# Kernel optimization log

Measured on AMD Instinct MI355X. Metric: run time of the kernel, lower is better.

The kernel has to match this reference:

```python
import jax, jax.numpy as jnp
import numpy as np
import math
from functools import partial

B = 256
H = 256
HEADS = 4
DK = H // HEADS
NA_MAX, NP_MAX, NH_MAX = 127, 23, 11


def _counts():
    i = np.arange(B)
    ac = (64 + i % 64).astype(np.int32)   # atoms per graph, 64..127
    pc = (8 + i % 16).astype(np.int32)    # pharm fragments per graph, 8..23
    hc = (4 + i % 8).astype(np.int32)     # hyper-edges per graph, 4..11
    return ac, pc, hc


def setup_inputs() -> dict:
    key = jax.random.key(0)
    ks = jax.random.split(key, 32)
    ac, pc, hc = _counts()
    na, npm, nh = int(ac.sum()), int(pc.sum()), int(hc.sum())
    w = 1.0 / math.sqrt(H)
    inp = {
        'atom_message': jax.random.normal(ks[0], (na, H), jnp.float32),
        'pharm_message': jax.random.normal(ks[1], (npm, H), jnp.float32),
        'hyper_message': jax.random.normal(ks[2], (nh, H), jnp.float32),
        'atom_counts': jnp.asarray(ac),
        'pharm_counts': jnp.asarray(pc),
        'hyper_counts': jnp.asarray(hc),
    }
    # two MultiHeadedAttention blocks: q/k/v/out linears each (W stored as [in, out])
    names = []
    for pre in ('p2h', 'a2p'):
        for part in ('Wq', 'bq', 'Wk', 'bk', 'Wv', 'bv', 'Wo', 'bo'):
            names.append(f'{pre}_{part}')
    ki = 3
    for n in names:
        if n.split('_')[1].startswith('W'):
            inp[n] = jax.random.normal(ks[ki], (H, H), jnp.float32) * w
        else:
            inp[n] = jax.random.normal(ks[ki], (H,), jnp.float32) * 0.01
        ki += 1
    # bidirectional GRU params, torch layout: W_ih [3H, H], W_hh [3H, H], b [3H]
    for d in ('f', 'b'):
        inp[f'gru_Wih_{d}'] = jax.random.normal(ks[ki], (3 * H, H), jnp.float32) * w; ki += 1
        inp[f'gru_Whh_{d}'] = jax.random.normal(ks[ki], (3 * H, H), jnp.float32) * w; ki += 1
        inp[f'gru_bih_{d}'] = jax.random.normal(ks[ki], (3 * H,), jnp.float32) * 0.01; ki += 1
        inp[f'gru_bhh_{d}'] = jax.random.normal(ks[ki], (3 * H,), jnp.float32) * 0.01; ki += 1
    return inp


def _split_pad(msg, counts, max_n):
    # faithful vectorized version of split_batch: narrow + zero-pad per graph
    starts = jnp.concatenate([jnp.zeros((1,), jnp.int32), jnp.cumsum(counts)[:-1].astype(jnp.int32)])
    j = jnp.arange(max_n)
    valid = j[None, :] < counts[:, None]                       # [B, max_n]
    idx = jnp.where(valid, starts[:, None] + j[None, :], msg.shape[0])
    padded_src = jnp.concatenate([msg, jnp.zeros((1, msg.shape[1]), msg.dtype)], 0)
    return padded_src[idx], valid                              # [B, max_n, H]


def _mha(q, k, v, mask, Wq, bq, Wk, bk, Wv, bv, Wo, bo):
    Bq, Lq, _ = q.shape
    def proj(x, W, b):
        y = x @ W + b
        return y.reshape(x.shape[0], x.shape[1], HEADS, DK).transpose(0, 2, 1, 3)
    qh, kh, vh = proj(q, Wq, bq), proj(k, Wk, bk), proj(v, Wv, bv)
    scores = jnp.einsum('bhqd,bhkd->bhqk', qh, kh) / math.sqrt(DK)
    scores = jnp.where(mask[:, None], jnp.float32(-1e9), scores)
    p = jax.nn.softmax(scores, axis=-1)
    o = jnp.einsum('bhqk,bhkd->bhqd', p, vh)
    o = o.transpose(0, 2, 1, 3).reshape(Bq, Lq, H)
    return o @ Wo + bo


def _gru_dir(x, h0, Wih, Whh, bih, bhh):
    # x: [B, T, H], torch GRU cell equations
    def step(h, xt):
        gi = xt @ Wih.T + bih
        gh = h @ Whh.T + bhh
        ir, iz, inn = jnp.split(gi, 3, axis=-1)
        hr, hz, hn = jnp.split(gh, 3, axis=-1)
        r = jax.nn.sigmoid(ir + hr)
        z = jax.nn.sigmoid(iz + hz)
        n = jnp.tanh(inn + r * hn)
        h = (1.0 - z) * n + z * h
        return h, h
    _, ys = jax.lax.scan(step, h0, x.transpose(1, 0, 2))
    return ys.transpose(1, 0, 2)


def reference(atom_message, pharm_message, hyper_message,
              p2h_Wq, p2h_bq, p2h_Wk, p2h_bk, p2h_Wv, p2h_bv, p2h_Wo, p2h_bo,
              a2p_Wq, a2p_bq, a2p_Wk, a2p_bk, a2p_Wv, a2p_bv, a2p_Wo, a2p_bo,
              gru_Wih_f, gru_Whh_f, gru_bih_f, gru_bhh_f,
              gru_Wih_b, gru_Whh_b, gru_bih_b, gru_bhh_b,
              atom_counts, pharm_counts, hyper_counts):
    atom_f, atom_valid = _split_pad(atom_message, atom_counts, NA_MAX)
    pharm_f, _ = _split_pad(pharm_message, pharm_counts, NP_MAX)
    hyper_f, _ = _split_pad(hyper_message, hyper_counts, NH_MAX)

    nz = lambda t: (t != 0).astype(jnp.float32)
    mask1 = jnp.einsum('bqh,bkh->bqk', nz(pharm_f), nz(hyper_f)) == 0  # [B, Np, Nh]
    mask2 = jnp.einsum('bqh,bkh->bqk', nz(atom_f), nz(pharm_f)) == 0   # [B, Na, Np]

    pharm_f = _mha(pharm_f, hyper_f, hyper_f, mask1,
                   p2h_Wq, p2h_bq, p2h_Wk, p2h_bk, p2h_Wv, p2h_bv, p2h_Wo, p2h_bo) + pharm_f
    h = _mha(atom_f, pharm_f, pharm_f, mask2,
             a2p_Wq, a2p_bq, a2p_Wk, a2p_bk, a2p_Wv, a2p_bv, a2p_Wo, a2p_bo) + atom_f

    h0 = h.max(axis=1)  # initial hidden per direction
    hf = _gru_dir(h, h0, gru_Wih_f, gru_Whh_f, gru_bih_f, gru_bhh_f)
    hb = _gru_dir(h[:, ::-1], h0, gru_Wih_b, gru_Whh_b, gru_bih_b, gru_bhh_b)[:, ::-1]
    hcat = jnp.concatenate([hf, hb], axis=-1)  # [B, Na, 2H]

    v = atom_valid.astype(hcat.dtype)[..., None]
    graph_embed = (hcat * v).sum(axis=1) / atom_counts[:, None].astype(hcat.dtype)
    return graph_embed  # [B, 2H]
```

## Files before the change

### kernel.cpp

```cpp
#include <hip/hip_runtime.h>
#include <hip/hip_fp16.h>
#include <math.h>

#define NB 256
#define HDIM 256
#define NHEADS 4
#define DKH 64
#define LA 127
#define LP 23
#define LH 11

typedef _Float16 h2v __attribute__((ext_vector_type(2)));
typedef _Float16 f16x8 __attribute__((ext_vector_type(8)));
typedef float f32x4 __attribute__((ext_vector_type(4)));
union F4H { float4 f4; h2v h[4]; };

__device__ __forceinline__ float dot2acc(h2v a, h2v b, float c) {
#if __has_builtin(__builtin_amdgcn_fdot2)
  return __builtin_amdgcn_fdot2(a, b, c, false);
#else
  return c + (float)a[0] * (float)b[0] + (float)a[1] * (float)b[1];
#endif
}

__device__ __forceinline__ float sigm(float x) { return 1.0f / (1.0f + __expf(-x)); }
__device__ __forceinline__ float tanh_fast(float x) { return 2.0f / (1.0f + __expf(-2.0f * x)) - 1.0f; }

__global__ void k_scan(const int* __restrict__ ac, const int* __restrict__ pc,
                       const int* __restrict__ hc, int* __restrict__ sa,
                       int* __restrict__ sp, int* __restrict__ sh) {
  int t = threadIdx.x;
  if (t == 0) { int s = 0; for (int i = 0; i < NB; i++) { sa[i] = s; s += ac[i]; } }
  else if (t == 1) { int s = 0; for (int i = 0; i < NB; i++) { sp[i] = s; s += pc[i]; } }
  else if (t == 2) { int s = 0; for (int i = 0; i < NB; i++) { sh[i] = s; s += hc[i]; } }
}

__global__ void k_cvt2(const float* __restrict__ a, __half* __restrict__ oa,
                       const float* __restrict__ b, __half* __restrict__ ob, int n) {
  int i = blockIdx.x * blockDim.x + threadIdx.x;
  if (i < n) oa[i] = __float2half(a[i]);
  else if (i < 2 * n) ob[i - n] = __float2half(b[i - n]);
}

__global__ void k_wprep2(const float* __restrict__ srcA, __half* __restrict__ dstA,
                         const float* __restrict__ srcB, __half* __restrict__ dstB) {
  const int NT = 768 * 256;
  int d0 = blockIdx.x * blockDim.x + threadIdx.x;
  const float* src = d0 < NT ? srcA : srcB;
  __half* dst = d0 < NT ? dstA : dstB;
  int d = d0 < NT ? d0 : d0 - NT;
  if (d0 >= 2 * NT) return;
  int u = d & 7;
  int lg = (d >> 3) & 3;
  int c = (d >> 5) % 768;
  int k0b = (d >> 5) / 768;
  dst[d] = __float2half(src[(size_t)c * 256 + k0b * 32 + lg * 8 + u]);
}

template <bool GATHER_A, bool RES_GATHER>
__global__ __launch_bounds__(256) void k_gemm(
    const float* __restrict__ A, const float* __restrict__ msg,
    const int* __restrict__ starts, const int* __restrict__ counts, int L,
    const float* __restrict__ W, const float* __restrict__ bias,
    const float* __restrict__ resmsg, float* __restrict__ C,
    __half* __restrict__ Ch, int N) {
  const int K = HDIM;
  __shared__ float As[16][76];
  __shared__ float Ws[16][72];
  int tid = threadIdx.x;
  int row0 = blockIdx.x * 64, col0 = blockIdx.y * 64;
  int arow = row0 + (tid >> 2);
  const float* asrc;
  if constexpr (GATHER_A) {
    int b = arow / L, t = arow - b * L;
    asrc = (t < counts[b]) ? (msg + (size_t)(starts[b] + t) * K) : nullptr;
  } else {
    asrc = A + (size_t)arow * K;
  }
  int ak = (tid & 3) * 4;
  int wk = tid >> 4, wn = (tid & 15) * 4;
  int ty = tid >> 4, tx = tid & 15;
  float acc[4][4] = {};
  for (int k0 = 0; k0 < K; k0 += 16) {
    float4 av = make_float4(0.f, 0.f, 0.f, 0.f);
    if (asrc) av = *(const float4*)(asrc + k0 + ak);
    float4 wv = *(const float4*)(W + (size_t)(k0 + wk) * N + col0 + wn);
    __syncthreads();
    int m = tid >> 2;
    As[ak + 0][m] = av.x; As[ak + 1][m] = av.y;
    As[ak + 2][m] = av.z; As[ak + 3][m] = av.w;
    *(float4*)&Ws[wk][wn] = wv;
    __syncthreads();
#pragma unroll
    for (int kk = 0; kk < 16; kk++) {
      float4 a = *(const float4*)&As[kk][ty * 4];
      float4 b = *(const float4*)&Ws[kk][tx * 4];
      acc[0][0] += a.x * b.x; acc[0][1] += a.x * b.y; acc[0][2] += a.x * b.z; acc[0][3] += a.x * b.w;
      acc[1][0] += a.y * b.x; acc[1][1] += a.y * b.y; acc[1][2] += a.y * b.z; acc[1][3] += a.y * b.w;
      acc[2][0] += a.z * b.x; acc[2][1] += a.z * b.y; acc[2][2] += a.z * b.z; acc[2][3] += a.z * b.w;
      acc[3][0] += a.w * b.x; acc[3][1] += a.w * b.y; acc[3][2] += a.w * b.z; acc[3][3] += a.w * b.w;
    }
  }
  float4 bv = *(const float4*)(bias + col0 + tx * 4);
#pragma unroll
  for (int i = 0; i < 4; i++) {
    int r = row0 + ty * 4 + i;
    float o0 = acc[i][0] + bv.x, o1 = acc[i][1] + bv.y,
          o2 = acc[i][2] + bv.z, o3 = acc[i][3] + bv.w;
    if constexpr (RES_GATHER) {
      int b = r / L, t = r - b * L;
      if (t < counts[b]) {
        float4 rv = *(const float4*)(resmsg + (size_t)(starts[b] + t) * K + col0 + tx * 4);
        o0 += rv.x; o1 += rv.y; o2 += rv.z; o3 += rv.w;
      }
    }
    size_t o = (size_t)r * N + col0 + tx * 4;
    *(float4*)(C + o) = make_float4(o0, o1, o2, o3);
    if (Ch) {
      Ch[o] = __float2half(o0); Ch[o + 1] = __float2half(o1);
      Ch[o + 2] = __float2half(o2); Ch[o + 3] = __float2half(o3);
    }
  }
}

template <bool GATHER_A>
__global__ __launch_bounds__(256) void k_gemm_kv(
    const float* __restrict__ A, const float* __restrict__ msg,
    const int* __restrict__ starts, const int* __restrict__ counts, int L,
    const float* __restrict__ W0, const float* __restrict__ b0, float* __restrict__ C0,
    const float* __restrict__ W1, const float* __restrict__ b1, float* __restrict__ C1) {
  const int K = HDIM, N = HDIM;
  const float* W = blockIdx.z ? W1 : W0;
  const float* bias = blockIdx.z ? b1 : b0;
  float* C = blockIdx.z ? C1 : C0;
  __shared__ float As[16][76];
  __shared__ float Ws[16][72];
  int tid = threadIdx.x;
  int row0 = blockIdx.x * 64, col0 = blockIdx.y * 64;
  int arow = row0 + (tid >> 2);
  const float* asrc;
  if constexpr (GATHER_A) {
    int b = arow / L, t = arow - b * L;
    asrc = (t < counts[b]) ? (msg + (size_t)(starts[b] + t) * K) : nullptr;
  } else {
    asrc = A + (size_t)arow * K;
  }
  int ak = (tid & 3) * 4;
  int wk = tid >> 4, wn = (tid & 15) * 4;
  int ty = tid >> 4, tx = tid & 15;
  float acc[4][4] = {};
  for (int k0 = 0; k0 < K; k0 += 16) {
    float4 av = make_float4(0.f, 0.f, 0.f, 0.f);
    if (asrc) av = *(const float4*)(asrc + k0 + ak);
    float4 wv = *(const float4*)(W + (size_t)(k0 + wk) * N + col0 + wn);
    __syncthreads();
    int m = tid >> 2;
    As[ak + 0][m] = av.x; As[ak + 1][m] = av.y;
    As[ak + 2][m] = av.z; As[ak + 3][m] = av.w;
    *(float4*)&Ws[wk][wn] = wv;
    __syncthreads();
#pragma unroll
    for (int kk = 0; kk < 16; kk++) {
      float4 a = *(const float4*)&As[kk][ty * 4];
      float4 b = *(const float4*)&Ws[kk][tx * 4];
      acc[0][0] += a.x * b.x; acc[0][1] += a.x * b.y; acc[0][2] += a.x * b.z; acc[0][3] += a.x * b.w;
      acc[1][0] += a.y * b.x; acc[1][1] += a.y * b.y; acc[1][2] += a.y * b.z; acc[1][3] += a.y * b.w;
      acc[2][0] += a.z * b.x; acc[2][1] += a.z * b.y; acc[2][2] += a.z * b.z; acc[2][3] += a.z * b.w;
      acc[3][0] += a.w * b.x; acc[3][1] += a.w * b.y; acc[3][2] += a.w * b.z; acc[3][3] += a.w * b.w;
    }
  }
  float4 bv = *(const float4*)(bias + col0 + tx * 4);
#pragma unroll
  for (int i = 0; i < 4; i++) {
    int r = row0 + ty * 4 + i;
    size_t o = (size_t)r * N + col0 + tx * 4;
    *(float4*)(C + o) = make_float4(acc[i][0] + bv.x, acc[i][1] + bv.y,
                                    acc[i][2] + bv.z, acc[i][3] + bv.w);
  }
}

__global__ __launch_bounds__(256) void k_mfma_gi2(
    const __half* __restrict__ A16,
    const __half* __restrict__ Wf_f, const __half* __restrict__ Wf_b,
    const float* __restrict__ bias_f, const float* __restrict__ bias_b,
    __half* __restrict__ Out_f, __half* __restrict__ Out_b) {
  const int N = 768;
  int y = blockIdx.y;
  const __half* Wf = y < 12 ? Wf_f : Wf_b;
  const float* bias = y < 12 ? bias_f : bias_b;
  __half* Out = y < 12 ? Out_f : Out_b;
  int col0 = (y < 12 ? y : y - 12) * 64;
  int w = threadIdx.x >> 6, l = threadIdx.x & 63;
  int row0 = blockIdx.x * 64 + w * 16;
  int lr = l & 15, lg = l >> 4;
  f32x4 acc[4] = {};
  const __half* arow = A16 + (size_t)(row0 + lr) * 256 + lg * 8;
#pragma unroll
  for (int k0b = 0; k0b < 8; k0b++) {
    f16x8 a = *(const f16x8*)(arow + k0b * 32);
#pragma unroll
    for (int nt = 0; nt < 4; nt++) {
      int c = col0 + nt * 16 + lr;
      f16x8 b = *(const f16x8*)(Wf + ((size_t)(k0b * N + c) * 4 + lg) * 8);
      acc[nt] = __builtin_amdgcn_mfma_f32_16x16x32_f16(a, b, acc[nt], 0, 0, 0);
    }
  }
#pragma unroll
  for (int nt = 0; nt < 4; nt++) {
    int c = col0 + nt * 16 + lr;
    float bv = bias[c];
#pragma unroll
    for (int r = 0; r < 4; r++) {
      int row = row0 + lg * 4 + r;
      Out[(size_t)row * N + c] = __float2half(acc[nt][r] + bv);
    }
  }
}

template <int LQ, int LK>
__global__ __launch_bounds__(128) void k_attn(
    float* __restrict__ q, const float* __restrict__ kbuf,
    const float* __restrict__ vbuf, const int* __restrict__ cq,
    const int* __restrict__ ck) {
  __shared__ float qs[LQ][65];
  __shared__ float ks[LK][65];
  __shared__ float vs[LK][65];
  int b = blockIdx.x, head = blockIdx.y;
  int tid = threadIdx.x;
  for (int idx = tid; idx < LQ * 16; idx += 128) {
    int i = idx >> 4, c = (idx & 15) * 4;
    float4 v = *(const float4*)(q + (size_t)(b * LQ + i) * HDIM + head * DKH + c);
    qs[i][c] = v.x; qs[i][c + 1] = v.y; qs[i][c + 2] = v.z; qs[i][c + 3] = v.w;
  }
  for (int idx = tid; idx < LK * 16; idx += 128) {
    int i = idx >> 4, c = (idx & 15) * 4;
    float4 v = *(const float4*)(kbuf + (size_t)(b * LK + i) * HDIM + head * DKH + c);
    ks[i][c] = v.x; ks[i][c + 1] = v.y; ks[i][c + 2] = v.z; ks[i][c + 3] = v.w;
    float4 w = *(const float4*)(vbuf + (size_t)(b * LK + i) * HDIM + head * DKH + c);
    vs[i][c] = w.x; vs[i][c + 1] = w.y; vs[i][c + 2] = w.z; vs[i][c + 3] = w.w;
  }
  __syncthreads();
  int nq = cq[b], nk = ck[b];
  for (int i = tid; i < LQ; i += 128) {
    float s[LK];
    float mx = -INFINITY;
    bool qv = i < nq;
#pragma unroll
    for (int k = 0; k < LK; k++) {
      float d = -1e9f;
      if (qv && k < nk) {
        float acc = 0.f;
        for (int c = 0; c < DKH; c++) acc += qs[i][c] * ks[k][c];
        d = acc * 0.125f;
      }
      s[k] = d;
      mx = fmaxf(mx, d);
    }
    float den = 0.f;
#pragma unroll
    for (int k = 0; k < LK; k++) { s[k] = expf(s[k] - mx); den += s[k]; }
    float inv = 1.0f / den;
    for (int c = 0; c < DKH; c++) {
      float acc = 0.f;
#pragma unroll
      for (int k = 0; k < LK; k++) acc += s[k] * vs[k][c];
      q[(size_t)(b * LQ + i) * HDIM + head * DKH + c] = acc * inv;
    }
  }
}

__global__ void k_rowmax(const float* __restrict__ h, float* __restrict__ h0) {
  int b = blockIdx.x, j = threadIdx.x;
  float m = -INFINITY;
  for (int t = 0; t < LA; t++) m = fmaxf(m, h[((size_t)b * LA + t) * HDIM + j]);
  h0[b * HDIM + j] = m;
}

__global__ __launch_bounds__(512, 2) void k_gru4(
    const float* __restrict__ h0, const __half* __restrict__ Wh_f,
    const __half* __restrict__ Wh_b, const __half* __restrict__ gi_f,
    const __half* __restrict__ gi_b, const float* __restrict__ bhh_f,
    const float* __restrict__ bhh_b, const int* __restrict__ ac,
    float* __restrict__ out) {
  int bid = blockIdx.x;
  int dir = bid & 1, pair = bid >> 1;
  int g0 = pair, g1 = pair + 128;
  int tid = threadIdx.x;
  int j = tid >> 1, half = tid & 1;
  const __half* W = dir ? Wh_b : Wh_f;
  const __half* gih = dir ? gi_b : gi_f;
  const float* bhh = dir ? bhh_b : bhh_f;

  F4H wr[16], wz[16], wn[16];
  {
    const float4* Wr4 = (const float4*)(W + (size_t)j * 256 + half * 128);
    const float4* Wz4 = (const float4*)(W + (size_t)(256 + j) * 256 + half * 128);
    const float4* Wn4 = (const float4*)(W + (size_t)(512 + j) * 256 + half * 128);
#pragma unroll
    for (int p = 0; p < 16; p++) wr[p].f4 = Wr4[p];
#pragma unroll
    for (int p = 0; p < 16; p++) wz[p].f4 = Wz4[p];
#pragma unroll
    for (int p = 0; p < 16; p++) wn[p].f4 = Wn4[p];
  }
  float br = bhh[j], bz = bhh[256 + j], bn = bhh[512 + j];
  int cnt = ac[g0];

  __shared__ __align__(16) __half hs[2][HDIM];
  float hprev0 = h0[(size_t)g0 * HDIM + j];
  float hprev1 = h0[(size_t)g1 * HDIM + j];
  if (half == 0) {
    hs[0][j] = __float2half(hprev0);
    hs[1][j] = __float2half(hprev1);
  }
  __syncthreads();

  const float4* h0p = (const float4*)hs[0] + half * 16;
  const float4* h1p = (const float4*)hs[1] + half * 16;
  float sum0 = 0.f, sum1 = 0.f;
  int nsteps = dir ? LA : cnt;
  for (int ti = 0; ti < nsteps; ti++) {
    int t = dir ? (LA - 1 - ti) : ti;
    const __half* gp0 = gih + ((size_t)g0 * LA + t) * 768 + j;
    const __half* gp1 = gih + ((size_t)g1 * LA + t) * 768 + j;
    float gr0 = __half2float(gp0[0]);
    float gz0 = __half2float(gp0[256]);
    float gn0 = __half2float(gp0[512]);
    float gr1 = __half2float(gp1[0]);
    float gz1 = __half2float(gp1[256]);
    float gn1 = __half2float(gp1[512]);
    float ap0 = 0.f, zp0 = 0.f, np0 = 0.f;
    float ap1 = 0.f, zp1 = 0.f, np1 = 0.f;
#pragma unroll
    for (int q = 0; q < 16; q++) {
      F4H hv0; hv0.f4 = h0p[q];
      F4H hv1; hv1.f4 = h1p[q];
#pragma unroll
      for (int u = 0; u < 4; u++) {
        ap0 = dot2acc(hv0.h[u], wr[q].h[u], ap0);
        zp0 = dot2acc(hv0.h[u], wz[q].h[u], zp0);
        np0 = dot2acc(hv0.h[u], wn[q].h[u], np0);
        ap1 = dot2acc(hv1.h[u], wr[q].h[u], ap1);
        zp1 = dot2acc(hv1.h[u], wz[q].h[u], zp1);
        np1 = dot2acc(hv1.h[u], wn[q].h[u], np1);
      }
    }
    ap0 += __shfl_xor(ap0, 1);
    zp0 += __shfl_xor(zp0, 1);
    np0 += __shfl_xor(np0, 1);
    ap1 += __shfl_xor(ap1, 1);
    zp1 += __shfl_xor(zp1, 1);
    np1 += __shfl_xor(np1, 1);
    float r0 = sigm(gr0 + br + ap0);
    float z0 = sigm(gz0 + bz + zp0);
    float n0 = tanh_fast(gn0 + bn + r0 * np0);
    float hnew0 = (1.f - z0) * n0 + z0 * hprev0;
    float r1 = sigm(gr1 + br + ap1);
    float z1 = sigm(gz1 + bz + zp1);
    float n1 = tanh_fast(gn1 + bn + r1 * np1);
    float hnew1 = (1.f - z1) * n1 + z1 * hprev1;
    __syncthreads();
    if (half == 0) {
      hs[0][j] = __float2half(hnew0);
      hs[1][j] = __float2half(hnew1);
    }
    hprev0 = hnew0;
    hprev1 = hnew1;
    if (t < cnt) { sum0 += hnew0; sum1 += hnew1; }
    __syncthreads();
  }
  if (half == 0) {
    out[(size_t)g0 * 512 + dir * 256 + j] = sum0 / (float)cnt;
    out[(size_t)g1 * 512 + dir * 256 + j] = sum1 / (float)cnt;
  }
}

extern "C" void kernel_launch(void* const* d_in, const int* in_sizes, int n_in,
                              void* d_out, int out_size, void* d_ws, size_t ws_size,
                              hipStream_t stream) {
  const float* atom_msg  = (const float*)d_in[0];
  const float* pharm_msg = (const float*)d_in[1];
  const float* hyper_msg = (const float*)d_in[2];
  const int* ac = (const int*)d_in[3];
  const int* pc = (const int*)d_in[4];
  const int* hc = (const int*)d_in[5];
  const float* p2h_Wq = (const float*)d_in[6];
  const float* p2h_bq = (const float*)d_in[7];
  const float* p2h_Wk = (const float*)d_in[8];
  const float* p2h_bk = (const float*)d_in[9];
  const float* p2h_Wv = (const float*)d_in[10];
  const float* p2h_bv = (const float*)d_in[11];
  const float* p2h_Wo = (const float*)d_in[12];
  const float* p2h_bo = (const float*)d_in[13];
  const float* a2p_Wq = (const float*)d_in[14];
  const float* a2p_bq = (const float*)d_in[15];
  const float* a2p_Wk = (const float*)d_in[16];
  const float* a2p_bk = (const float*)d_in[17];
  const float* a2p_Wv = (const float*)d_in[18];
  const float* a2p_bv = (const float*)d_in[19];
  const float* a2p_Wo = (const float*)d_in[20];
  const float* a2p_bo = (const float*)d_in[21];
  const float* Wih_f  = (const float*)d_in[22];
  const float* Whh_f  = (const float*)d_in[23];
  const float* bih_f  = (const float*)d_in[24];
  const float* bhh_f  = (const float*)d_in[25];
  const float* Wih_b  = (const float*)d_in[26];
  const float* Whh_b  = (const float*)d_in[27];
  const float* bih_b  = (const float*)d_in[28];
  const float* bhh_b  = (const float*)d_in[29];
  float* out = (float*)d_out;
  (void)in_sizes; (void)n_in; (void)out_size; (void)ws_size;

  char* wsb = (char*)d_ws;
  size_t off = 0;
  auto alloc = [&](size_t bytes) -> void* {
    void* p = wsb + off;
    off += (bytes + 255) & ~(size_t)255;
    return p;
  };
  const int MA = NB * LA, MP = NB * LP, MH = NB * LH;
  int* sa = (int*)alloc(NB * 4);
  int* sp = (int*)alloc(NB * 4);
  int* sh = (int*)alloc(NB * 4);
  __half* Wh16_f = (__half*)alloc((size_t)768 * 256 * 2);
  __half* Wh16_b = (__half*)alloc((size_t)768 * 256 * 2);
  __half* Wf16_f = (__half*)alloc((size_t)768 * 256 * 2);
  __half* Wf16_b = (__half*)alloc((size_t)768 * 256 * 2);
  float* q_p = (float*)alloc((size_t)MP * HDIM * 4);
  float* k_h = (float*)alloc((size_t)MH * HDIM * 4);
  float* v_h = (float*)alloc((size_t)MH * HDIM * 4);
  float* ph2 = (float*)alloc((size_t)MP * HDIM * 4);
  float* q_a = (float*)alloc((size_t)MA * HDIM * 4);
  float* k_p = (float*)alloc((size_t)MP * HDIM * 4);
  float* v_p = (float*)alloc((size_t)MP * HDIM * 4);
  float* h_x = (float*)alloc((size_t)MA * HDIM * 4);
  __half* h_x16 = (__half*)alloc((size_t)MA * HDIM * 2);
  float* h0  = (float*)alloc((size_t)NB * HDIM * 4);
  __half* gi_f = (__half*)alloc((size_t)MA * 768 * 2);
  __half* gi_b = (__half*)alloc((size_t)MA * 768 * 2);

  k_scan<<<1, 64, 0, stream>>>(ac, pc, hc, sa, sp, sh);
  int tb = (768 * 256 + 255) / 256;
  k_cvt2<<<2 * tb, 256, 0, stream>>>(Whh_f, Wh16_f, Whh_b, Wh16_b, 768 * 256);
  k_wprep2<<<2 * tb, 256, 0, stream>>>(Wih_f, Wf16_f, Wih_b, Wf16_b);

  k_gemm<true, false><<<dim3(MP / 64, 4), 256, 0, stream>>>(
      nullptr, pharm_msg, sp, pc, LP, p2h_Wq, p2h_bq, nullptr, q_p, nullptr, 256);
  k_gemm_kv<true><<<dim3(MH / 64, 4, 2), 256, 0, stream>>>(
      nullptr, hyper_msg, sh, hc, LH, p2h_Wk, p2h_bk, k_h, p2h_Wv, p2h_bv, v_h);
  k_attn<LP, LH><<<dim3(NB, NHEADS), 128, 0, stream>>>(q_p, k_h, v_h, pc, hc);
  k_gemm<false, true><<<dim3(MP / 64, 4), 256, 0, stream>>>(
      q_p, nullptr, sp, pc, LP, p2h_Wo, p2h_bo, pharm_msg, ph2, nullptr, 256);

  k_gemm<true, false><<<dim3(MA / 64, 4), 256, 0, stream>>>(
      nullptr, atom_msg, sa, ac, LA, a2p_Wq, a2p_bq, nullptr, q_a, nullptr, 256);
  k_gemm_kv<false><<<dim3(MP / 64, 4, 2), 256, 0, stream>>>(
      ph2, nullptr, nullptr, nullptr, 1, a2p_Wk, a2p_bk, k_p, a2p_Wv, a2p_bv, v_p);
  k_attn<LA, LP><<<dim3(NB, NHEADS), 128, 0, stream>>>(q_a, k_p, v_p, ac, pc);
  k_gemm<false, true><<<dim3(MA / 64, 4), 256, 0, stream>>>(
      q_a, nullptr, sa, ac, LA, a2p_Wo, a2p_bo, atom_msg, h_x, h_x16, 256);

  k_rowmax<<<NB, 256, 0, stream>>>(h_x, h0);
  k_mfma_gi2<<<dim3(MA / 64, 24), 256, 0, stream>>>(
      h_x16, Wf16_f, Wf16_b, bih_f, bih_b, gi_f, gi_b);
  k_gru4<<<NB, 512, 0, stream>>>(h0, Wh16_f, Wh16_b, gi_f, gi_b, bhh_f, bhh_b, ac, out);
}
```

Baseline: 756.6 us.

## Merge prep kernels, fuse Q/K/V projections, fold rowmax into gate GEMM

Merges the scan and the two weight-conversion kernels into one prep launch. Folds the separate Q and K/V projection GEMMs of each attention block into one three-slice launch, with row-range early exit for the shorter slices. Runs the per-graph row max as an extra grid row of the input-gate MFMA kernel instead of a separate kernel. The aim is fewer kernel launches and more concurrent blocks, at the cost of runtime branching in place of templates and many idle early-exit blocks.

```diff
diff --git a/kernel.cpp b/kernel.cpp
--- a/kernel.cpp
+++ b/kernel.cpp
@@ -26,35 +26,37 @@
 __device__ __forceinline__ float sigm(float x) { return 1.0f / (1.0f + __expf(-x)); }
 __device__ __forceinline__ float tanh_fast(float x) { return 2.0f / (1.0f + __expf(-2.0f * x)) - 1.0f; }
 
-__global__ void k_scan(const int* __restrict__ ac, const int* __restrict__ pc,
+__global__ void k_prep(const int* __restrict__ ac, const int* __restrict__ pc,
                        const int* __restrict__ hc, int* __restrict__ sa,
-                       int* __restrict__ sp, int* __restrict__ sh) {
-  int t = threadIdx.x;
-  if (t == 0) { int s = 0; for (int i = 0; i < NB; i++) { sa[i] = s; s += ac[i]; } }
-  else if (t == 1) { int s = 0; for (int i = 0; i < NB; i++) { sp[i] = s; s += pc[i]; } }
-  else if (t == 2) { int s = 0; for (int i = 0; i < NB; i++) { sh[i] = s; s += hc[i]; } }
-}
-
-__global__ void k_cvt2(const float* __restrict__ a, __half* __restrict__ oa,
-                       const float* __restrict__ b, __half* __restrict__ ob, int n) {
-  int i = blockIdx.x * blockDim.x + threadIdx.x;
-  if (i < n) oa[i] = __float2half(a[i]);
-  else if (i < 2 * n) ob[i - n] = __float2half(b[i - n]);
-}
-
-__global__ void k_wprep2(const float* __restrict__ srcA, __half* __restrict__ dstA,
-                         const float* __restrict__ srcB, __half* __restrict__ dstB) {
+                       int* __restrict__ sp, int* __restrict__ sh,
+                       const float* __restrict__ Whh_f, __half* __restrict__ Wh16_f,
+                       const float* __restrict__ Whh_b, __half* __restrict__ Wh16_b,
+                       const float* __restrict__ Wih_f, __half* __restrict__ Wf16_f,
+                       const float* __restrict__ Wih_b, __half* __restrict__ Wf16_b) {
   const int NT = 768 * 256;
-  int d0 = blockIdx.x * blockDim.x + threadIdx.x;
-  const float* src = d0 < NT ? srcA : srcB;
-  __half* dst = d0 < NT ? dstA : dstB;
-  int d = d0 < NT ? d0 : d0 - NT;
-  if (d0 >= 2 * NT) return;
-  int u = d & 7;
-  int lg = (d >> 3) & 3;
-  int c = (d >> 5) % 768;
-  int k0b = (d >> 5) / 768;
-  dst[d] = __float2half(src[(size_t)c * 256 + k0b * 32 + lg * 8 + u]);
+  if (blockIdx.x == gridDim.x - 1) {
+    int t = threadIdx.x;
+    if (t == 0) { int s = 0; for (int i = 0; i < NB; i++) { sa[i] = s; s += ac[i]; } }
+    else if (t == 1) { int s = 0; for (int i = 0; i < NB; i++) { sp[i] = s; s += pc[i]; } }
+    else if (t == 2) { int s = 0; for (int i = 0; i < NB; i++) { sh[i] = s; s += hc[i]; } }
+    return;
+  }
+  int idx = blockIdx.x * 256 + threadIdx.x;
+  if (idx < NT) { Wh16_f[idx] = __float2half(Whh_f[idx]); return; }
+  idx -= NT;
+  if (idx < NT) { Wh16_b[idx] = __float2half(Whh_b[idx]); return; }
+  idx -= NT;
+  if (idx < NT) {
+    int u = idx & 7, lg = (idx >> 3) & 3, c = (idx >> 5) % 768, k0b = (idx >> 5) / 768;
+    Wf16_f[idx] = __float2half(Wih_f[(size_t)c * 256 + k0b * 32 + lg * 8 + u]);
+    return;
+  }
+  idx -= NT;
+  if (idx < NT) {
+    int u = idx & 7, lg = (idx >> 3) & 3, c = (idx >> 5) % 768, k0b = (idx >> 5) / 768;
+    Wf16_b[idx] = __float2half(Wih_b[(size_t)c * 256 + k0b * 32 + lg * 8 + u]);
+    return;
+  }
 }
 
 template <bool GATHER_A, bool RES_GATHER>
@@ -123,25 +125,30 @@
   }
 }
 
-template <bool GATHER_A>
-__global__ __launch_bounds__(256) void k_gemm_kv(
-    const float* __restrict__ A, const float* __restrict__ msg,
-    const int* __restrict__ starts, const int* __restrict__ counts, int L,
-    const float* __restrict__ W0, const float* __restrict__ b0, float* __restrict__ C0,
-    const float* __restrict__ W1, const float* __restrict__ b1, float* __restrict__ C1) {
+__global__ __launch_bounds__(256) void k_gemm_qkv(
+    const float* A0, const int* st0, const int* ct0, int L0, int g0, int nr0,
+    const float* W0, const float* b0, float* C0,
+    const float* A1, const int* st1, const int* ct1, int L1, int g1, int nr1,
+    const float* W1, const float* b1, float* C1,
+    const float* A2, const int* st2, const int* ct2, int L2, int g2, int nr2,
+    const float* W2, const float* b2, float* C2) {
   const int K = HDIM, N = HDIM;
-  const float* W = blockIdx.z ? W1 : W0;
-  const float* bias = blockIdx.z ? b1 : b0;
-  float* C = blockIdx.z ? C1 : C0;
+  int z = blockIdx.z;
+  const float* A; const int* starts; const int* counts; int L, gat, nrows;
+  const float* W; const float* bias; float* C;
+  if (z == 0)      { A = A0; starts = st0; counts = ct0; L = L0; gat = g0; nrows = nr0; W = W0; bias = b0; C = C0; }
+  else if (z == 1) { A = A1; starts = st1; counts = ct1; L = L1; gat = g1; nrows = nr1; W = W1; bias = b1; C = C1; }
+  else             { A = A2; starts = st2; counts = ct2; L = L2; gat = g2; nrows = nr2; W = W2; bias = b2; C = C2; }
+  int row0 = blockIdx.x * 64, col0 = blockIdx.y * 64;
+  if (row0 >= nrows) return;
   __shared__ float As[16][76];
   __shared__ float Ws[16][72];
   int tid = threadIdx.x;
-  int row0 = blockIdx.x * 64, col0 = blockIdx.y * 64;
   int arow = row0 + (tid >> 2);
   const float* asrc;
-  if constexpr (GATHER_A) {
+  if (gat) {
     int b = arow / L, t = arow - b * L;
-    asrc = (t < counts[b]) ? (msg + (size_t)(starts[b] + t) * K) : nullptr;
+    asrc = (t < counts[b]) ? (A + (size_t)(starts[b] + t) * K) : nullptr;
   } else {
     asrc = A + (size_t)arow * K;
   }
@@ -183,9 +190,19 @@
     const __half* __restrict__ A16,
     const __half* __restrict__ Wf_f, const __half* __restrict__ Wf_b,
     const float* __restrict__ bias_f, const float* __restrict__ bias_b,
-    __half* __restrict__ Out_f, __half* __restrict__ Out_b) {
+    __half* __restrict__ Out_f, __half* __restrict__ Out_b,
+    const float* __restrict__ h_x, float* __restrict__ h0) {
   const int N = 768;
   int y = blockIdx.y;
+  if (y == 24) {
+    int b = blockIdx.x;
+    if (b >= NB) return;
+    int j = threadIdx.x;
+    float m = -INFINITY;
+    for (int t = 0; t < LA; t++) m = fmaxf(m, h_x[((size_t)b * LA + t) * HDIM + j]);
+    h0[b * HDIM + j] = m;
+    return;
+  }
   const __half* Wf = y < 12 ? Wf_f : Wf_b;
   const float* bias = y < 12 ? bias_f : bias_b;
   __half* Out = y < 12 ? Out_f : Out_b;
@@ -267,13 +284,6 @@
       q[(size_t)(b * LQ + i) * HDIM + head * DKH + c] = acc * inv;
     }
   }
-}
-
-__global__ void k_rowmax(const float* __restrict__ h, float* __restrict__ h0) {
-  int b = blockIdx.x, j = threadIdx.x;
-  float m = -INFINITY;
-  for (int t = 0; t < LA; t++) m = fmaxf(m, h[((size_t)b * LA + t) * HDIM + j]);
-  h0[b * HDIM + j] = m;
 }
 
 __global__ __launch_bounds__(512, 2) void k_gru4(
@@ -439,29 +449,30 @@
   __half* gi_f = (__half*)alloc((size_t)MA * 768 * 2);
   __half* gi_b = (__half*)alloc((size_t)MA * 768 * 2);
 
-  k_scan<<<1, 64, 0, stream>>>(ac, pc, hc, sa, sp, sh);
-  int tb = (768 * 256 + 255) / 256;
-  k_cvt2<<<2 * tb, 256, 0, stream>>>(Whh_f, Wh16_f, Whh_b, Wh16_b, 768 * 256);
-  k_wprep2<<<2 * tb, 256, 0, stream>>>(Wih_f, Wf16_f, Wih_b, Wf16_b);
-
-  k_gemm<true, false><<<dim3(MP / 64, 4), 256, 0, stream>>>(
-      nullptr, pharm_msg, sp, pc, LP, p2h_Wq, p2h_bq, nullptr, q_p, nullptr, 256);
-  k_gemm_kv<true><<<dim3(MH / 64, 4, 2), 256, 0, stream>>>(
-      nullptr, hyper_msg, sh, hc, LH, p2h_Wk, p2h_bk, k_h, p2h_Wv, p2h_bv, v_h);
+  {
+    const int NT = 768 * 256;
+    int blocks = 4 * NT / 256 + 1;
+    k_prep<<<blocks, 256, 0, stream>>>(ac, pc, hc, sa, sp, sh,
+        Whh_f, Wh16_f, Whh_b, Wh16_b, Wih_f, Wf16_f, Wih_b, Wf16_b);
+  }
+
+  k_gemm_qkv<<<dim3(MP / 64, 4, 3), 256, 0, stream>>>(
+      pharm_msg, sp, pc, LP, 1, MP, p2h_Wq, p2h_bq, q_p,
+      hyper_msg, sh, hc, LH, 1, MH, p2h_Wk, p2h_bk, k_h,
+      hyper_msg, sh, hc, LH, 1, MH, p2h_Wv, p2h_bv, v_h);
   k_attn<LP, LH><<<dim3(NB, NHEADS), 128, 0, stream>>>(q_p, k_h, v_h, pc, hc);
   k_gemm<false, true><<<dim3(MP / 64, 4), 256, 0, stream>>>(
       q_p, nullptr, sp, pc, LP, p2h_Wo, p2h_bo, pharm_msg, ph2, nullptr, 256);
 
-  k_gemm<true, false><<<dim3(MA / 64, 4), 256, 0, stream>>>(
-      nullptr, atom_msg, sa, ac, LA, a2p_Wq, a2p_bq, nullptr, q_a, nullptr, 256);
-  k_gemm_kv<false><<<dim3(MP / 64, 4, 2), 256, 0, stream>>>(
-      ph2, nullptr, nullptr, nullptr, 1, a2p_Wk, a2p_bk, k_p, a2p_Wv, a2p_bv, v_p);
+  k_gemm_qkv<<<dim3(MA / 64, 4, 3), 256, 0, stream>>>(
+      atom_msg, sa, ac, LA, 1, MA, a2p_Wq, a2p_bq, q_a,
+      ph2, nullptr, nullptr, 1, 0, MP, a2p_Wk, a2p_bk, k_p,
+      ph2, nullptr, nullptr, 1, 0, MP, a2p_Wv, a2p_bv, v_p);
   k_attn<LA, LP><<<dim3(NB, NHEADS), 128, 0, stream>>>(q_a, k_p, v_p, ac, pc);
   k_gemm<false, true><<<dim3(MA / 64, 4), 256, 0, stream>>>(
       q_a, nullptr, sa, ac, LA, a2p_Wo, a2p_bo, atom_msg, h_x, h_x16, 256);
 
-  k_rowmax<<<NB, 256, 0, stream>>>(h_x, h0);
-  k_mfma_gi2<<<dim3(MA / 64, 24), 256, 0, stream>>>(
-      h_x16, Wf16_f, Wf16_b, bih_f, bih_b, gi_f, gi_b);
+  k_mfma_gi2<<<dim3(MA / 64, 25), 256, 0, stream>>>(
+      h_x16, Wf16_f, Wf16_b, bih_f, bih_b, gi_f, gi_b, h_x, h0);
   k_gru4<<<NB, 512, 0, stream>>>(h0, Wh16_f, Wh16_b, gi_f, gi_b, bhh_f, bhh_b, ac, out);
 }
```

Measured after the change: 739.5 us, median of 2. -2.3%, faster.
